# Kernel tuning notes

Measured on AMD Instinct MI355X. Metric: run time of the kernel, lower is better.

The kernel has to match this reference:

```python
import jax, jax.numpy as jnp
import numpy as np

N = 100000
IN_CH = 128
OUT_CH = 128
E = 1600000


def setup_inputs() -> dict:
    key = jax.random.key(0)
    k1, k2, k3, k4 = jax.random.split(key, 4)
    x = jax.random.normal(k1, (N, IN_CH), dtype=jnp.float32)
    edge_index = jax.random.randint(k2, (2, E), 0, N, dtype=jnp.int64)
    # Glorot-style init for the GCNConv linear weight, zero bias (PyG default)
    W = jax.random.normal(k3, (IN_CH, OUT_CH), dtype=jnp.float32) * (1.0 / np.sqrt(IN_CH))
    b = jnp.zeros((OUT_CH,), dtype=jnp.float32)
    return {"x": x, "edge_index": edge_index, "W": W, "b": b}


def reference(x, edge_index, W, b):
    n = x.shape[0]
    # ---- add self loops (PyG GCNConv default add_self_loops=True) ----
    loops = jnp.arange(n, dtype=edge_index.dtype)
    row = jnp.concatenate([edge_index[0], loops])  # source
    col = jnp.concatenate([edge_index[1], loops])  # target
    # ---- symmetric degree normalization: D^{-1/2} (A+I) D^{-1/2} ----
    ones = jnp.ones(col.shape[0], dtype=x.dtype)
    deg = jax.ops.segment_sum(ones, col, num_segments=n)  # in-degree incl. self loop
    deg_inv_sqrt = jnp.where(deg > 0, jax.lax.rsqrt(deg), 0.0)
    norm = deg_inv_sqrt[row] * deg_inv_sqrt[col]  # [E+N]
    # ---- linear transform then gather-scale-scatter aggregation ----
    h = x @ W  # [N, OUT_CH]
    msgs = norm[:, None] * h[row]  # [E+N, OUT_CH]
    out = jax.ops.segment_sum(msgs, col, num_segments=n) + b  # [N, OUT_CH]
    # ---- ReLU ----
    return jax.nn.relu(out)
```

## Files before the change

### kernel.cpp

```cpp
#include <hip/hip_runtime.h>
#include <hip/hip_bf16.h>
#include <hip/hip_fp16.h>

#define IN_CH 128
#define OUT_CH 128
#define TM 64
#define CHUNK 8192
#define NPB 512
#define BSHIFT 9
#define CPAD 16
#define CAPT 16384

typedef __attribute__((ext_vector_type(8))) short short8;
typedef __attribute__((ext_vector_type(4))) float f32x4;

__device__ __forceinline__ unsigned short f2bf(float f) {
    union { float f; unsigned u; } v; v.f = f;
    unsigned r = v.u + 0x7FFFu + ((v.u >> 16) & 1u);
    return (unsigned short)(r >> 16);
}


__global__ __launch_bounds__(256) void init_kernel(int* __restrict__ cursor, int NBK) {
    int t = threadIdx.x;
    if (t < NBK) cursor[t * CPAD] = t * CAPT;
}

__global__ __launch_bounds__(256) void partition_kernel(const int* __restrict__ row,
                                                        const int* __restrict__ col,
                                                        int* __restrict__ cursor,
                                                        int* __restrict__ tmp,
                                                        int E, int NBK, int vec) {
    __shared__ int lcnt[256];
    __shared__ int lstart[256];
    __shared__ int lbase[256];
    __shared__ int lscan[256];
    __shared__ int buf[CHUNK];
    __shared__ unsigned char bid[CHUNK];
    int t = threadIdx.x;
    int base = blockIdx.x * CHUNK;
    int nloc = min(CHUNK, E - base);
    lcnt[t] = 0;
    __syncthreads();
    if (vec) {
        const int4* c4 = (const int4*)(col + base);
        int nv = nloc >> 2;
        for (int i = t; i < nv; i += 256) {
            int4 c = c4[i];
            atomicAdd(&lcnt[c.x >> BSHIFT], 1);
            atomicAdd(&lcnt[c.y >> BSHIFT], 1);
            atomicAdd(&lcnt[c.z >> BSHIFT], 1);
            atomicAdd(&lcnt[c.w >> BSHIFT], 1);
        }
        for (int i = (nv << 2) + t; i < nloc; i += 256)
            atomicAdd(&lcnt[col[base + i] >> BSHIFT], 1);
    } else {
        for (int i = t; i < nloc; i += 256)
            atomicAdd(&lcnt[col[base + i] >> BSHIFT], 1);
    }
    __syncthreads();
    int v = lcnt[t];
    lscan[t] = v;
    __syncthreads();
    for (int off = 1; off < 256; off <<= 1) {
        int a = lscan[t];
        int b2 = (t >= off) ? lscan[t - off] : 0;
        __syncthreads();
        lscan[t] = a + b2;
        __syncthreads();
    }
    int excl = lscan[t] - v;
    lstart[t] = excl;
    lcnt[t] = excl;
    lbase[t] = (t < NBK && v) ? atomicAdd(&cursor[t * CPAD], v) : 0;
    __syncthreads();
    if (vec) {
        const int4* c4 = (const int4*)(col + base);
        const int4* r4 = (const int4*)(row + base);
        int nv = nloc >> 2;
        for (int i = t; i < nv; i += 256) {
            int4 c = c4[i];
            int4 r = r4[i];
            int b0 = c.x >> BSHIFT, p0 = atomicAdd(&lcnt[b0], 1);
            buf[p0] = r.x | ((c.x & (NPB - 1)) << 20); bid[p0] = (unsigned char)b0;
            int b1 = c.y >> BSHIFT, p1 = atomicAdd(&lcnt[b1], 1);
            buf[p1] = r.y | ((c.y & (NPB - 1)) << 20); bid[p1] = (unsigned char)b1;
            int b2 = c.z >> BSHIFT, p2 = atomicAdd(&lcnt[b2], 1);
            buf[p2] = r.z | ((c.z & (NPB - 1)) << 20); bid[p2] = (unsigned char)b2;
            int b3 = c.w >> BSHIFT, p3 = atomicAdd(&lcnt[b3], 1);
            buf[p3] = r.w | ((c.w & (NPB - 1)) << 20); bid[p3] = (unsigned char)b3;
        }
        for (int i = (nv << 2) + t; i < nloc; i += 256) {
            int c = col[base + i], r = row[base + i];
            int b = c >> BSHIFT, p = atomicAdd(&lcnt[b], 1);
            buf[p] = r | ((c & (NPB - 1)) << 20); bid[p] = (unsigned char)b;
        }
    } else {
        for (int i = t; i < nloc; i += 256) {
            int c = col[base + i], r = row[base + i];
            int b = c >> BSHIFT, p = atomicAdd(&lcnt[b], 1);
            buf[p] = r | ((c & (NPB - 1)) << 20); bid[p] = (unsigned char)b;
        }
    }
    __syncthreads();
    for (int i = t; i < nloc; i += 256) {
        int b = bid[i];
        int gidx = lbase[b] + (i - lstart[b]);
        if (gidx < (b + 1) * CAPT) tmp[gidx] = buf[i];
    }
}

__global__ __launch_bounds__(256) void cscan_kernel(const int* __restrict__ cursor,
                                                    int* __restrict__ bstart,
                                                    int* __restrict__ offs,
                                                    int NBK, int N) {
    __shared__ int tsum[256];
    int t = threadIdx.x;
    int v = (t < NBK) ? min(cursor[t * CPAD] - t * CAPT, CAPT) : 0;
    tsum[t] = v;
    __syncthreads();
    for (int off = 1; off < 256; off <<= 1) {
        int a = tsum[t];
        int b2 = (t >= off) ? tsum[t - off] : 0;
        __syncthreads();
        tsum[t] = a + b2;
        __syncthreads();
    }
    int excl = tsum[t] - v;
    if (t < NBK) bstart[t] = excl;
    if (t == 255) { bstart[NBK] = tsum[255]; offs[N] = tsum[255]; }
}

__global__ __launch_bounds__(256) void csr_build_kernel(const int* __restrict__ tmp,
                                                        const int* __restrict__ cursor,
                                                        const int* __restrict__ bstart,
                                                        int* __restrict__ offs,
                                                        float* __restrict__ dis,
                                                        int* __restrict__ srcs, int N) {
    __shared__ int cnt[NPB];
    __shared__ int cur[NPB];
    int b = blockIdx.x;
    int t = threadIdx.x;
    int wbeg = b * CAPT;
    int cnt_b = min(cursor[b * CPAD] - wbeg, CAPT);
    int cbeg = bstart[b];
    cnt[2 * t] = 0;
    cnt[2 * t + 1] = 0;
    __syncthreads();
    for (int e = t; e < cnt_b; e += 256)
        atomicAdd(&cnt[(tmp[wbeg + e] >> 20)], 1);
    __syncthreads();
    int v0 = cnt[2 * t], v1 = cnt[2 * t + 1];
    int s = v0 + v1;
    cur[t] = s;
    __syncthreads();
    for (int off = 1; off < 256; off <<= 1) {
        int a = cur[t];
        int b2 = (t >= off) ? cur[t - off] : 0;
        __syncthreads();
        cur[t] = a + b2;
        __syncthreads();
    }
    int excl_pair = cur[t] - s;
    __syncthreads();
    int e0 = excl_pair;
    int e1 = excl_pair + v0;
    cur[2 * t] = e0;
    cur[2 * t + 1] = e1;
    int n0 = b * NPB + 2 * t;
    int n1 = n0 + 1;
    if (n0 < N) { offs[n0] = cbeg + e0; dis[n0] = rsqrtf((float)(v0 + 1)); }
    if (n1 < N) { offs[n1] = cbeg + e1; dis[n1] = rsqrtf((float)(v1 + 1)); }
    __syncthreads();
    for (int e = t; e < cnt_b; e += 256) {
        int p = tmp[wbeg + e];
        int slot = atomicAdd(&cur[p >> 20], 1);
        srcs[cbeg + slot] = p & 0xFFFFF;
    }
}

__global__ __launch_bounds__(256) void gemm_mfma_kernel(const float* __restrict__ A,
        const float* __restrict__ W, const float* __restrict__ dis,
        __half* __restrict__ G, int n) {
    __shared__ unsigned short Bf[16384];
    __shared__ unsigned short As[64 * 136];
    int t = threadIdx.x;
    const float4* W4 = (const float4*)W;
#pragma unroll
    for (int rep = 0; rep < 16; ++rep) {
        int idx4 = rep * 256 + t;
        float4 v = W4[idx4];
        int lin = idx4 * 4;
        int k = lin >> 7;
        int n0 = lin & 127;
        int ks = k >> 5;
        int kk = k & 31;
        int quad = kk >> 3;
        int j = kk & 7;
#pragma unroll
        for (int e = 0; e < 4; ++e) {
            int nc = n0 + e;
            int ct = nc >> 4;
            int lane = (quad << 4) | (nc & 15);
            Bf[(((ct << 2) | ks) * 64 + lane) * 8 + j] = f2bf((&v.x)[e]);
        }
    }
    int row0 = blockIdx.x * TM;
    const float4* A4 = (const float4*)A;
#pragma unroll
    for (int rep = 0; rep < 8; ++rep) {
        int idx = rep * 256 + t;
        int r = idx >> 5;
        int c4 = idx & 31;
        int gr = row0 + r;
        float4 v = make_float4(0.f, 0.f, 0.f, 0.f);
        if (gr < n) v = A4[(size_t)gr * 32 + c4];
        ushort4 h;
        h.x = f2bf(v.x); h.y = f2bf(v.y); h.z = f2bf(v.z); h.w = f2bf(v.w);
        *(ushort4*)&As[r * 136 + c4 * 4] = h;
    }
    __syncthreads();
    int w = t >> 6;
    int lane = t & 63;
    int m = lane & 15;
    int quad = lane >> 4;
    short8 af[4];
#pragma unroll
    for (int ks = 0; ks < 4; ++ks)
        af[ks] = *(const short8*)&As[(w * 16 + m) * 136 + ks * 32 + quad * 8];
    int grow_base = row0 + w * 16 + quad * 4;
    float dsc[4];
#pragma unroll
    for (int reg = 0; reg < 4; ++reg)
        dsc[reg] = (grow_base + reg < n) ? dis[grow_base + reg] : 0.f;
#pragma unroll
    for (int ct = 0; ct < 8; ++ct) {
        f32x4 acc = {0.f, 0.f, 0.f, 0.f};
#pragma unroll
        for (int ks = 0; ks < 4; ++ks) {
            short8 bf = *(const short8*)&Bf[((ct * 4 + ks) * 64 + lane) * 8];
            acc = __builtin_amdgcn_mfma_f32_16x16x32_bf16(af[ks], bf, acc, 0, 0, 0);
        }
        int nc = ct * 16 + m;
#pragma unroll
        for (int reg = 0; reg < 4; ++reg) {
            int grow = grow_base + reg;
            if (grow < n)
                G[(size_t)grow * 128 + nc] = __float2half(dsc[reg] * acc[reg]);
        }
    }
}

__global__ __launch_bounds__(256) void gemm_g16_kernel(const float* __restrict__ A,
        const float* __restrict__ W, const float* __restrict__ dis,
        __half* __restrict__ G, int n) {
    __shared__ __half Wh[128 * 128];
    __shared__ float As[TM * 128];
    int t = threadIdx.x;
    const float4* W4 = (const float4*)W;
#pragma unroll
    for (int j = 0; j < 16; ++j) {
        int idx = t + 256 * j;
        float4 v = W4[idx];
        __half2 p0 = __floats2half2_rn(v.x, v.y);
        __half2 p1 = __floats2half2_rn(v.z, v.w);
        *(__half2*)&Wh[idx * 4]     = p0;
        *(__half2*)&Wh[idx * 4 + 2] = p1;
    }
    int row0 = blockIdx.x * TM;
    const float4* A4 = (const float4*)A;
#pragma unroll
    for (int j = 0; j < 8; ++j) {
        int idx = t + 256 * j;
        int r = idx >> 5;
        int c4 = idx & 31;
        int gr = row0 + r;
        float4 v = make_float4(0.f, 0.f, 0.f, 0.f);
        if (gr < n) v = A4[(size_t)gr * 32 + c4];
        *(float4*)&As[r * 128 + c4 * 4] = v;
    }
    __syncthreads();
    int tcol = t & 15;
    int trow = t >> 4;
    int cb = tcol * 8;
    float acc[4][8];
#pragma unroll
    for (int r = 0; r < 4; ++r)
#pragma unroll
        for (int c = 0; c < 8; ++c) acc[r][c] = 0.f;
    const float* Abase = &As[(trow * 4) * 128];
#pragma unroll 4
    for (int k = 0; k < 128; ++k) {
        float4 wv = *(const float4*)&Wh[k * 128 + cb];
        const __half2* wh = (const __half2*)&wv;
        float2 w01 = __half22float2(wh[0]);
        float2 w23 = __half22float2(wh[1]);
        float2 w45 = __half22float2(wh[2]);
        float2 w67 = __half22float2(wh[3]);
        float wreg[8] = {w01.x, w01.y, w23.x, w23.y, w45.x, w45.y, w67.x, w67.y};
#pragma unroll
        for (int r = 0; r < 4; ++r) {
            float a = Abase[r * 128 + k];
#pragma unroll
            for (int c = 0; c < 8; ++c) acc[r][c] = fmaf(a, wreg[c], acc[r][c]);
        }
    }
#pragma unroll
    for (int r = 0; r < 4; ++r) {
        int gr = row0 + trow * 4 + r;
        if (gr < n) {
            float dsc2 = dis[gr];
            __half2 o[4];
#pragma unroll
            for (int j = 0; j < 4; ++j)
                o[j] = __floats2half2_rn(dsc2 * acc[r][2 * j], dsc2 * acc[r][2 * j + 1]);
            *(float4*)&G[(size_t)gr * 128 + cb] = *(float4*)o;
        }
    }
}

__global__ __launch_bounds__(256) void aggregate_g16_kernel(
        const __half2* __restrict__ g2, const int* __restrict__ srcs,
        const int* __restrict__ offs, const float* __restrict__ dis,
        const float* __restrict__ bias, float2* __restrict__ out2, int n) {
    int gid = blockIdx.x * blockDim.x + threadIdx.x;
    int wid = gid >> 6;
    int lane = gid & 63;
    if (wid >= n) return;
    int beg = offs[wid];
    int end = offs[wid + 1];
    float di = dis[wid];
    float2 xi = __half22float2(g2[(size_t)wid * 64 + lane]);
    float accx = xi.x;
    float accy = xi.y;
    int e = beg;
    for (; e + 8 <= end; e += 8) {
        int s0 = srcs[e],     s1 = srcs[e + 1], s2 = srcs[e + 2], s3 = srcs[e + 3];
        int s4 = srcs[e + 4], s5 = srcs[e + 5], s6 = srcs[e + 6], s7 = srcs[e + 7];
        float2 v0 = __half22float2(g2[(size_t)s0 * 64 + lane]);
        float2 v1 = __half22float2(g2[(size_t)s1 * 64 + lane]);
        float2 v2 = __half22float2(g2[(size_t)s2 * 64 + lane]);
        float2 v3 = __half22float2(g2[(size_t)s3 * 64 + lane]);
        float2 v4 = __half22float2(g2[(size_t)s4 * 64 + lane]);
        float2 v5 = __half22float2(g2[(size_t)s5 * 64 + lane]);
        float2 v6 = __half22float2(g2[(size_t)s6 * 64 + lane]);
        float2 v7 = __half22float2(g2[(size_t)s7 * 64 + lane]);
        accx += ((v0.x + v1.x) + (v2.x + v3.x)) + ((v4.x + v5.x) + (v6.x + v7.x));
        accy += ((v0.y + v1.y) + (v2.y + v3.y)) + ((v4.y + v5.y) + (v6.y + v7.y));
    }
    for (; e + 4 <= end; e += 4) {
        int s0 = srcs[e], s1 = srcs[e + 1], s2 = srcs[e + 2], s3 = srcs[e + 3];
        float2 v0 = __half22float2(g2[(size_t)s0 * 64 + lane]);
        float2 v1 = __half22float2(g2[(size_t)s1 * 64 + lane]);
        float2 v2 = __half22float2(g2[(size_t)s2 * 64 + lane]);
        float2 v3 = __half22float2(g2[(size_t)s3 * 64 + lane]);
        accx += (v0.x + v1.x) + (v2.x + v3.x);
        accy += (v0.y + v1.y) + (v2.y + v3.y);
    }
    for (; e < end; ++e) {
        float2 v = __half22float2(g2[(size_t)srcs[e] * 64 + lane]);
        accx += v.x;
        accy += v.y;
    }
    float2 bv = ((const float2*)bias)[lane];
    float2 r;
    r.x = fmaxf(fmaf(di, accx, bv.x), 0.f);
    r.y = fmaxf(fmaf(di, accy, bv.y), 0.f);
    out2[(size_t)wid * 64 + lane] = r;
}

__global__ void count_kernel(const int* __restrict__ col, int* __restrict__ deg, int E) {
    int i = blockIdx.x * blockDim.x + threadIdx.x;
    if (i < E) atomicAdd(&deg[col[i]], 1);
}

__global__ void scan_block_kernel(const int* __restrict__ in, int* __restrict__ out,
                                  int* __restrict__ bsums, float* __restrict__ dis, int n) {
    __shared__ int lds[256];
    int t = threadIdx.x;
    int base = blockIdx.x * 1024;
    int v[4];
    int idx = base + t * 4;
#pragma unroll
    for (int j = 0; j < 4; ++j) v[j] = (idx + j < n) ? in[idx + j] : 0;
#pragma unroll
    for (int j = 0; j < 4; ++j)
        if (idx + j < n) dis[idx + j] = rsqrtf((float)(v[j] + 1));
    int sum = v[0] + v[1] + v[2] + v[3];
    lds[t] = sum;
    __syncthreads();
    for (int off = 1; off < 256; off <<= 1) {
        int a = lds[t];
        int bq = (t >= off) ? lds[t - off] : 0;
        __syncthreads();
        lds[t] = a + bq;
        __syncthreads();
    }
    int run = (t == 0) ? 0 : lds[t - 1];
    if (t == 255 && bsums) bsums[blockIdx.x] = lds[255];
#pragma unroll
    for (int j = 0; j < 4; ++j) {
        if (idx + j < n) out[idx + j] = run;
        run += v[j];
    }
}

__global__ void scan_sums_kernel(int* __restrict__ bsums, int nB) {
    __shared__ int lds[256];
    int t = threadIdx.x;
    lds[t] = (t < nB) ? bsums[t] : 0;
    __syncthreads();
    for (int off = 1; off < 256; off <<= 1) {
        int a = lds[t];
        int bq = (t >= off) ? lds[t - off] : 0;
        __syncthreads();
        lds[t] = a + bq;
        __syncthreads();
    }
    if (t < nB) bsums[t] = (t == 0) ? 0 : lds[t - 1];
}

__global__ void scan_add_kernel(int* __restrict__ offs, const int* __restrict__ bsums,
                                int n, int total) {
    int i = blockIdx.x * blockDim.x + threadIdx.x;
    if (i < n) offs[i] += bsums[i >> 10];
    if (i == 0) offs[n] = total;
}

__global__ void fill_kernel(const int* __restrict__ row, const int* __restrict__ col,
                            const int* __restrict__ offs, int* __restrict__ deg,
                            int* __restrict__ srcs, int E) {
    int i = blockIdx.x * blockDim.x + threadIdx.x;
    if (i < E) {
        int c = col[i];
        int old = atomicSub(&deg[c], 1);
        srcs[offs[c] + old - 1] = row[i];
    }
}

__global__ __launch_bounds__(256) void aggregate_f32_kernel(
        const float2* __restrict__ x2, const int* __restrict__ srcs,
        const int* __restrict__ offs, const float* __restrict__ dis,
        float2* __restrict__ out2, int n) {
    int gid = blockIdx.x * blockDim.x + threadIdx.x;
    int wid = gid >> 6;
    int lane = gid & 63;
    if (wid >= n) return;
    int beg = offs[wid];
    int end = offs[wid + 1];
    float di = dis[wid];
    float2 xi = x2[(size_t)wid * 64 + lane];
    float accx = di * xi.x;
    float accy = di * xi.y;
    for (int e = beg; e < end; ++e) {
        int s = srcs[e];
        float ds = dis[s];
        float2 xs = x2[(size_t)s * 64 + lane];
        accx = fmaf(ds, xs.x, accx);
        accy = fmaf(ds, xs.y, accy);
    }
    float2 r;
    r.x = di * accx;
    r.y = di * accy;
    out2[(size_t)wid * 64 + lane] = r;
}

__global__ __launch_bounds__(256) void gemm_inplace_kernel(float* __restrict__ io,
                                                           const float* __restrict__ W,
                                                           const float* __restrict__ bias, int n) {
    __shared__ float rowL[128];
    __shared__ float part[128];
    int t = threadIdx.x;
    int c = t & 127;
    int half = t >> 7;
    float w[64];
#pragma unroll
    for (int j = 0; j < 64; ++j) w[j] = W[(half * 64 + j) * 128 + c];
    float bv = bias[c];
    int kbase = half * 64;
    for (int r = blockIdx.x; r < n; r += gridDim.x) {
        if (t < 128) rowL[t] = io[(size_t)r * 128 + t];
        __syncthreads();
        float acc = 0.f;
#pragma unroll
        for (int j = 0; j < 64; ++j) acc = fmaf(rowL[kbase + j], w[j], acc);
        if (half) part[c] = acc;
        __syncthreads();
        if (!half) {
            float v = acc + part[c] + bv;
            io[(size_t)r * 128 + c] = fmaxf(v, 0.f);
        }
        __syncthreads();
    }
}

extern "C" void kernel_launch(void* const* d_in, const int* in_sizes, int n_in,
                              void* d_out, int out_size, void* d_ws, size_t ws_size,
                              hipStream_t stream) {
    const float* x  = (const float*)d_in[0];
    const int*   ei = (const int*)d_in[1];
    const float* W  = (const float*)d_in[2];
    const float* b  = (const float*)d_in[3];
    float* out = (float*)d_out;

    int N = in_sizes[0] / IN_CH;
    int E = in_sizes[1] / 2;
    const int* rowp = ei;
    const int* colp = ei + E;
    int NBK = (N + NPB - 1) >> BSHIFT;
    int tpb = 256;
    int nchunks = (E + CHUNK - 1) / CHUNK;

    char* p = (char*)d_ws;
    auto take = [&](size_t bytes) { char* q = p; p += (bytes + 255) & ~(size_t)255; return q; };
    int*    cursor = (int*)take((size_t)256 * CPAD * 4);
    int*    bstart = (int*)take((size_t)(NBK + 1) * 4);
    int*    offs   = (int*)take((size_t)(N + 1) * 4);
    float*  dis    = (float*)take((size_t)N * 4);
    int*    srcs   = (int*)take((size_t)E * 4);
    __half* g      = (__half*)take((size_t)N * 128 * 2);
    bool fast = (NBK <= 256) && ((size_t)(p - (char*)d_ws) <= ws_size) &&
                ((size_t)NBK * CAPT <= (size_t)out_size) && (N < (1 << 20)) &&
                ((size_t)E + NPB <= (size_t)CAPT * NBK);

    long long threads_agg = (long long)N * 64;
    int agg_blocks = (int)((threads_agg + tpb - 1) / tpb);

    if (fast) {
        int* tmp = (int*)d_out;
        int vec = (((uintptr_t)colp | (uintptr_t)rowp) & 15) == 0 ? 1 : 0;
        init_kernel<<<1, 256, 0, stream>>>(cursor, NBK);
        partition_kernel<<<nchunks, 256, 0, stream>>>(rowp, colp, cursor, tmp, E, NBK, vec);
        cscan_kernel<<<1, 256, 0, stream>>>(cursor, bstart, offs, NBK, N);
        csr_build_kernel<<<NBK, 256, 0, stream>>>(tmp, cursor, bstart, offs, dis, srcs, N);
        gemm_mfma_kernel<<<(N + TM - 1) / TM, 256, 0, stream>>>(x, W, dis, g, N);
        aggregate_g16_kernel<<<agg_blocks, tpb, 0, stream>>>(
            (const __half2*)g, srcs, offs, dis, b, (float2*)out, N);
    } else {
        char* q = (char*)d_ws;
        auto take2 = [&](size_t bytes) { char* r = q; q += (bytes + 255) & ~(size_t)255; return r; };
        int*    deg2   = (int*)take2((size_t)N * 4);
        int*    offs2  = (int*)take2((size_t)(N + 1) * 4);
        int*    bsums2 = (int*)take2(256 * 4);
        int*    srcs2  = (int*)take2((size_t)E * 4);
        float*  dis2   = (float*)take2((size_t)N * 4);
        __half* g2b    = (__half*)take2((size_t)N * 128 * 2);
        bool fits2 = ((size_t)(q - (char*)d_ws)) <= ws_size;
        hipMemsetAsync(deg2, 0, (size_t)N * 4, stream);
        count_kernel<<<(E + tpb - 1) / tpb, tpb, 0, stream>>>(colp, deg2, E);
        int nB = (N + 1023) / 1024;
        scan_block_kernel<<<nB, 256, 0, stream>>>(deg2, offs2, bsums2, dis2, N);
        scan_sums_kernel<<<1, 256, 0, stream>>>(bsums2, nB);
        scan_add_kernel<<<(N + tpb - 1) / tpb, tpb, 0, stream>>>(offs2, bsums2, N, E);
        fill_kernel<<<(E + tpb - 1) / tpb, tpb, 0, stream>>>(rowp, colp, offs2, deg2, srcs2, E);
        if (fits2) {
            gemm_g16_kernel<<<(N + TM - 1) / TM, 256, 0, stream>>>(x, W, dis2, g2b, N);
            aggregate_g16_kernel<<<agg_blocks, tpb, 0, stream>>>(
                (const __half2*)g2b, srcs2, offs2, dis2, b, (float2*)out, N);
        } else {
            aggregate_f32_kernel<<<agg_blocks, tpb, 0, stream>>>(
                (const float2*)x, srcs2, offs2, dis2, (float2*)out, N);
            gemm_inplace_kernel<<<2048, 256, 0, stream>>>(out, W, b, N);
        }
    }
}
```

Measured before the change: 248.2 us.

## Fold block scan into CSR build, prepack W once, stream A directly into MFMA

```diff
diff --git a/kernel.cpp b/kernel.cpp
--- a/kernel.cpp
+++ b/kernel.cpp
@@ -13,6 +13,7 @@
 
 typedef __attribute__((ext_vector_type(8))) short short8;
 typedef __attribute__((ext_vector_type(4))) float f32x4;
+typedef __attribute__((ext_vector_type(2))) float f32x2;
 
 __device__ __forceinline__ unsigned short f2bf(float f) {
     union { float f; unsigned u; } v; v.f = f;
@@ -30,6 +31,8 @@
                                                         const int* __restrict__ col,
                                                         int* __restrict__ cursor,
                                                         int* __restrict__ tmp,
+                                                        const float* __restrict__ W,
+                                                        unsigned short* __restrict__ Wf,
                                                         int E, int NBK, int vec) {
     __shared__ int lcnt[256];
     __shared__ int lstart[256];
@@ -38,6 +41,19 @@
     __shared__ int buf[CHUNK];
     __shared__ unsigned char bid[CHUNK];
     int t = threadIdx.x;
+    if (blockIdx.x == gridDim.x - 1) {
+        for (int idx = t; idx < 16384; idx += 256) {
+            int j = idx & 7;
+            int lane = (idx >> 3) & 63;
+            int ctks = idx >> 9;
+            int ks = ctks & 3;
+            int ct = ctks >> 2;
+            int k = ks * 32 + (lane >> 4) * 8 + j;
+            int nc = ct * 16 + (lane & 15);
+            Wf[idx] = f2bf(W[k * 128 + nc]);
+        }
+        return;
+    }
     int base = blockIdx.x * CHUNK;
     int nloc = min(CHUNK, E - base);
     lcnt[t] = 0;
@@ -110,43 +126,33 @@
     }
 }
 
-__global__ __launch_bounds__(256) void cscan_kernel(const int* __restrict__ cursor,
-                                                    int* __restrict__ bstart,
-                                                    int* __restrict__ offs,
-                                                    int NBK, int N) {
-    __shared__ int tsum[256];
-    int t = threadIdx.x;
-    int v = (t < NBK) ? min(cursor[t * CPAD] - t * CAPT, CAPT) : 0;
-    tsum[t] = v;
-    __syncthreads();
-    for (int off = 1; off < 256; off <<= 1) {
-        int a = tsum[t];
-        int b2 = (t >= off) ? tsum[t - off] : 0;
-        __syncthreads();
-        tsum[t] = a + b2;
-        __syncthreads();
-    }
-    int excl = tsum[t] - v;
-    if (t < NBK) bstart[t] = excl;
-    if (t == 255) { bstart[NBK] = tsum[255]; offs[N] = tsum[255]; }
-}
-
 __global__ __launch_bounds__(256) void csr_build_kernel(const int* __restrict__ tmp,
                                                         const int* __restrict__ cursor,
-                                                        const int* __restrict__ bstart,
                                                         int* __restrict__ offs,
                                                         float* __restrict__ dis,
-                                                        int* __restrict__ srcs, int N) {
+                                                        int* __restrict__ srcs,
+                                                        int N, int NBK) {
     __shared__ int cnt[NPB];
     __shared__ int cur[NPB];
+    __shared__ int bsum[256];
     int b = blockIdx.x;
     int t = threadIdx.x;
+    int cv = (t < NBK) ? min(cursor[t * CPAD] - t * CAPT, CAPT) : 0;
+    bsum[t] = cv;
+    cnt[2 * t] = 0;
+    cnt[2 * t + 1] = 0;
+    __syncthreads();
+    for (int off = 1; off < 256; off <<= 1) {
+        int a = bsum[t];
+        int b2 = (t >= off) ? bsum[t - off] : 0;
+        __syncthreads();
+        bsum[t] = a + b2;
+        __syncthreads();
+    }
     int wbeg = b * CAPT;
     int cnt_b = min(cursor[b * CPAD] - wbeg, CAPT);
-    int cbeg = bstart[b];
-    cnt[2 * t] = 0;
-    cnt[2 * t + 1] = 0;
-    __syncthreads();
+    int cbeg = bsum[b] - cnt_b;
+    if (b == 0 && t == 0) offs[N] = bsum[NBK - 1];
     for (int e = t; e < cnt_b; e += 256)
         atomicAdd(&cnt[(tmp[wbeg + e] >> 20)], 1);
     __syncthreads();
@@ -180,65 +186,44 @@
 }
 
 __global__ __launch_bounds__(256) void gemm_mfma_kernel(const float* __restrict__ A,
-        const float* __restrict__ W, const float* __restrict__ dis,
+        const unsigned short* __restrict__ Wf, const float* __restrict__ dis,
         __half* __restrict__ G, int n) {
-    __shared__ unsigned short Bf[16384];
-    __shared__ unsigned short As[64 * 136];
-    int t = threadIdx.x;
-    const float4* W4 = (const float4*)W;
-#pragma unroll
-    for (int rep = 0; rep < 16; ++rep) {
-        int idx4 = rep * 256 + t;
-        float4 v = W4[idx4];
-        int lin = idx4 * 4;
-        int k = lin >> 7;
-        int n0 = lin & 127;
-        int ks = k >> 5;
-        int kk = k & 31;
-        int quad = kk >> 3;
-        int j = kk & 7;
-#pragma unroll
-        for (int e = 0; e < 4; ++e) {
-            int nc = n0 + e;
-            int ct = nc >> 4;
-            int lane = (quad << 4) | (nc & 15);
-            Bf[(((ct << 2) | ks) * 64 + lane) * 8 + j] = f2bf((&v.x)[e]);
-        }
-    }
-    int row0 = blockIdx.x * TM;
-    const float4* A4 = (const float4*)A;
-#pragma unroll
-    for (int rep = 0; rep < 8; ++rep) {
-        int idx = rep * 256 + t;
-        int r = idx >> 5;
-        int c4 = idx & 31;
-        int gr = row0 + r;
-        float4 v = make_float4(0.f, 0.f, 0.f, 0.f);
-        if (gr < n) v = A4[(size_t)gr * 32 + c4];
-        ushort4 h;
-        h.x = f2bf(v.x); h.y = f2bf(v.y); h.z = f2bf(v.z); h.w = f2bf(v.w);
-        *(ushort4*)&As[r * 136 + c4 * 4] = h;
-    }
-    __syncthreads();
+    int t = threadIdx.x;
     int w = t >> 6;
     int lane = t & 63;
     int m = lane & 15;
     int quad = lane >> 4;
+    int row = blockIdx.x * TM + w * 16 + m;
     short8 af[4];
-#pragma unroll
-    for (int ks = 0; ks < 4; ++ks)
-        af[ks] = *(const short8*)&As[(w * 16 + m) * 136 + ks * 32 + quad * 8];
-    int grow_base = row0 + w * 16 + quad * 4;
+    if (row < n) {
+        const f32x4* Ar = (const f32x4*)(A + (size_t)row * 128);
+#pragma unroll
+        for (int ks = 0; ks < 4; ++ks) {
+            f32x4 v0 = __builtin_nontemporal_load(Ar + ks * 8 + quad * 2);
+            f32x4 v1 = __builtin_nontemporal_load(Ar + ks * 8 + quad * 2 + 1);
+            short8 a;
+            a[0] = (short)f2bf(v0.x); a[1] = (short)f2bf(v0.y);
+            a[2] = (short)f2bf(v0.z); a[3] = (short)f2bf(v0.w);
+            a[4] = (short)f2bf(v1.x); a[5] = (short)f2bf(v1.y);
+            a[6] = (short)f2bf(v1.z); a[7] = (short)f2bf(v1.w);
+            af[ks] = a;
+        }
+    } else {
+#pragma unroll
+        for (int ks = 0; ks < 4; ++ks) af[ks] = (short8)0;
+    }
+    int grow_base = blockIdx.x * TM + w * 16 + quad * 4;
     float dsc[4];
 #pragma unroll
     for (int reg = 0; reg < 4; ++reg)
         dsc[reg] = (grow_base + reg < n) ? dis[grow_base + reg] : 0.f;
+    const short8* B8 = (const short8*)Wf;
 #pragma unroll
     for (int ct = 0; ct < 8; ++ct) {
         f32x4 acc = {0.f, 0.f, 0.f, 0.f};
 #pragma unroll
         for (int ks = 0; ks < 4; ++ks) {
-            short8 bf = *(const short8*)&Bf[((ct * 4 + ks) * 64 + lane) * 8];
+            short8 bf = B8[(ct * 4 + ks) * 64 + lane];
             acc = __builtin_amdgcn_mfma_f32_16x16x32_bf16(af[ks], bf, acc, 0, 0, 0);
         }
         int nc = ct * 16 + m;
@@ -335,8 +320,14 @@
     float accy = xi.y;
     int e = beg;
     for (; e + 8 <= end; e += 8) {
-        int s0 = srcs[e],     s1 = srcs[e + 1], s2 = srcs[e + 2], s3 = srcs[e + 3];
-        int s4 = srcs[e + 4], s5 = srcs[e + 5], s6 = srcs[e + 6], s7 = srcs[e + 7];
+        int s0 = __builtin_nontemporal_load(srcs + e);
+        int s1 = __builtin_nontemporal_load(srcs + e + 1);
+        int s2 = __builtin_nontemporal_load(srcs + e + 2);
+        int s3 = __builtin_nontemporal_load(srcs + e + 3);
+        int s4 = __builtin_nontemporal_load(srcs + e + 4);
+        int s5 = __builtin_nontemporal_load(srcs + e + 5);
+        int s6 = __builtin_nontemporal_load(srcs + e + 6);
+        int s7 = __builtin_nontemporal_load(srcs + e + 7);
         float2 v0 = __half22float2(g2[(size_t)s0 * 64 + lane]);
         float2 v1 = __half22float2(g2[(size_t)s1 * 64 + lane]);
         float2 v2 = __half22float2(g2[(size_t)s2 * 64 + lane]);
@@ -349,7 +340,10 @@
         accy += ((v0.y + v1.y) + (v2.y + v3.y)) + ((v4.y + v5.y) + (v6.y + v7.y));
     }
     for (; e + 4 <= end; e += 4) {
-        int s0 = srcs[e], s1 = srcs[e + 1], s2 = srcs[e + 2], s3 = srcs[e + 3];
+        int s0 = __builtin_nontemporal_load(srcs + e);
+        int s1 = __builtin_nontemporal_load(srcs + e + 1);
+        int s2 = __builtin_nontemporal_load(srcs + e + 2);
+        int s3 = __builtin_nontemporal_load(srcs + e + 3);
         float2 v0 = __half22float2(g2[(size_t)s0 * 64 + lane]);
         float2 v1 = __half22float2(g2[(size_t)s1 * 64 + lane]);
         float2 v2 = __half22float2(g2[(size_t)s2 * 64 + lane]);
@@ -358,15 +352,15 @@
         accy += (v0.y + v1.y) + (v2.y + v3.y);
     }
     for (; e < end; ++e) {
-        float2 v = __half22float2(g2[(size_t)srcs[e] * 64 + lane]);
+        float2 v = __half22float2(g2[(size_t)__builtin_nontemporal_load(srcs + e) * 64 + lane]);
         accx += v.x;
         accy += v.y;
     }
     float2 bv = ((const float2*)bias)[lane];
-    float2 r;
+    f32x2 r;
     r.x = fmaxf(fmaf(di, accx, bv.x), 0.f);
     r.y = fmaxf(fmaf(di, accy, bv.y), 0.f);
-    out2[(size_t)wid * 64 + lane] = r;
+    __builtin_nontemporal_store(r, (f32x2*)&out2[(size_t)wid * 64 + lane]);
 }
 
 __global__ void count_kernel(const int* __restrict__ col, int* __restrict__ deg, int E) {
@@ -514,11 +508,11 @@
     char* p = (char*)d_ws;
     auto take = [&](size_t bytes) { char* q = p; p += (bytes + 255) & ~(size_t)255; return q; };
     int*    cursor = (int*)take((size_t)256 * CPAD * 4);
-    int*    bstart = (int*)take((size_t)(NBK + 1) * 4);
     int*    offs   = (int*)take((size_t)(N + 1) * 4);
     float*  dis    = (float*)take((size_t)N * 4);
     int*    srcs   = (int*)take((size_t)E * 4);
     __half* g      = (__half*)take((size_t)N * 128 * 2);
+    unsigned short* Wf = (unsigned short*)take((size_t)16384 * 2);
     bool fast = (NBK <= 256) && ((size_t)(p - (char*)d_ws) <= ws_size) &&
                 ((size_t)NBK * CAPT <= (size_t)out_size) && (N < (1 << 20)) &&
                 ((size_t)E + NPB <= (size_t)CAPT * NBK);
@@ -530,10 +524,9 @@
         int* tmp = (int*)d_out;
         int vec = (((uintptr_t)colp | (uintptr_t)rowp) & 15) == 0 ? 1 : 0;
         init_kernel<<<1, 256, 0, stream>>>(cursor, NBK);
-        partition_kernel<<<nchunks, 256, 0, stream>>>(rowp, colp, cursor, tmp, E, NBK, vec);
-        cscan_kernel<<<1, 256, 0, stream>>>(cursor, bstart, offs, NBK, N);
-        csr_build_kernel<<<NBK, 256, 0, stream>>>(tmp, cursor, bstart, offs, dis, srcs, N);
-        gemm_mfma_kernel<<<(N + TM - 1) / TM, 256, 0, stream>>>(x, W, dis, g, N);
+        partition_kernel<<<nchunks + 1, 256, 0, stream>>>(rowp, colp, cursor, tmp, W, Wf, E, NBK, vec);
+        csr_build_kernel<<<NBK, 256, 0, stream>>>(tmp, cursor, offs, dis, srcs, N, NBK);
+        gemm_mfma_kernel<<<(N + TM - 1) / TM, 256, 0, stream>>>(x, Wf, dis, g, N);
         aggregate_g16_kernel<<<agg_blocks, tpb, 0, stream>>>(
             (const __half2*)g, srcs, offs, dis, b, (float2*)out, N);
     } else {
```

Result: faster. 236.8 us (-4.6%).
